# Optimization experiments

Hardware: AMD Instinct MI355X
Metric: run time of the kernel (lower is better)

Reference implementation:

```python
import jax, jax.numpy as jnp
import numpy as np

T, B, D, H = 1024, 128, 256, 256


def setup_inputs() -> dict:
    key = jax.random.key(0)
    ks = jax.random.split(key, 16)
    s_in = 1.0 / np.sqrt(D + H)  # torch Linear default init scale
    inp = {
        "inputs": jax.random.normal(ks[0], (T, B, D), dtype=jnp.float32),
        "Wf": jax.random.uniform(ks[1], (H, D + H), jnp.float32, -s_in, s_in),
        "bf": jax.random.uniform(ks[2], (H,), jnp.float32, -s_in, s_in),
        "Wi": jax.random.uniform(ks[3], (H, D + H), jnp.float32, -s_in, s_in),
        "bi": jax.random.uniform(ks[4], (H,), jnp.float32, -s_in, s_in),
        "Wg": jax.random.uniform(ks[5], (H, D + H), jnp.float32, -s_in, s_in),
        "bg": jax.random.uniform(ks[6], (H,), jnp.float32, -s_in, s_in),
        "Wo": jax.random.uniform(ks[7], (H, D + H), jnp.float32, -s_in, s_in),
        "bo": jax.random.uniform(ks[8], (H,), jnp.float32, -s_in, s_in),
        # estimator params stacked over the 4 gates (order: f, i, g, o)
        "estW1": jax.random.uniform(ks[9], (4, 8, H), jnp.float32, -1/np.sqrt(H), 1/np.sqrt(H)),
        "estb1": jax.random.uniform(ks[10], (4, 8), jnp.float32, -1/np.sqrt(H), 1/np.sqrt(H)),
        "estW2": jax.random.uniform(ks[11], (4, 4, 8), jnp.float32, -1/np.sqrt(8), 1/np.sqrt(8)),
        "estb2": jax.random.uniform(ks[12], (4, 4), jnp.float32, -1/np.sqrt(8), 1/np.sqrt(8)),
        "estW3": jax.random.uniform(ks[13], (4, 1, 4), jnp.float32, -0.5, 0.5),
        "estb3": jax.random.uniform(ks[14], (4, 1), jnp.float32, -0.5, 0.5),
    }
    return inp


def reference(inputs, Wf, bf, Wi, bi, Wg, bg, Wo, bo,
              estW1, estb1, estW2, estb2, estW3, estb3):
    def est(x, k):
        # tiny MLP: H -> 8 -> 4 -> 1 with tanh/tanh/sigmoid
        h1 = jnp.tanh(x @ estW1[k].T + estb1[k])
        h2 = jnp.tanh(h1 @ estW2[k].T + estb2[k])
        return jax.nn.sigmoid(h2 @ estW3[k].T + estb3[k])  # [B, 1]

    def step(carry, x):
        hx, cx = carry
        comb = jnp.concatenate([x, hx], axis=1)  # [B, D+H]
        f = jax.nn.sigmoid(comb @ Wf.T + bf)
        i = jax.nn.sigmoid(comb @ Wi.T + bi)
        g = jnp.tanh(comb @ Wg.T + bg)
        o = jax.nn.sigmoid(comb @ Wo.T + bo)
        f = f * est(f, 0)
        i = i * est(i, 1)
        g = g * est(g, 2)
        o = o * est(o, 3)
        cx = f * cx + i * g
        hx = o * jnp.tanh(cx)
        return (hx, cx), hx

    hx0 = jnp.zeros((B, H), dtype=inputs.dtype)
    cx0 = jnp.zeros((B, H), dtype=inputs.dtype)
    (hx, cx), stacked = jax.lax.scan(step, (hx0, cx0), inputs)
    return stacked, hx, cx
```

## Files before the change

### kernel.cpp

```cpp
#include <hip/hip_runtime.h>
#include <hip/hip_fp16.h>
#include <math.h>

#define T_STEPS 1024
#define BATCH   128
#define D_IN    256
#define H_DIM   256
#define NCOL    1024

typedef _Float16 half2_t __attribute__((ext_vector_type(2)));

__device__ __forceinline__ float sigmoidf_(float x) {
    return 1.0f / (1.0f + __expf(-x));
}

__device__ __forceinline__ float tanhf_(float x) {
    float ax = fabsf(x);
    float t = __expf(-2.0f * ax);
    float r = (1.0f - t) / (1.0f + t);
    return copysignf(r, x);
}

__device__ __forceinline__ float dot2f(unsigned int w, unsigned int h, float acc) {
#if __has_builtin(__builtin_amdgcn_fdot2)
    return __builtin_amdgcn_fdot2(__builtin_bit_cast(half2_t, w),
                                  __builtin_bit_cast(half2_t, h), acc, false);
#else
    __half2 wv = *(__half2*)&w, hv = *(__half2*)&h;
    acc = fmaf(__half2float(wv.x), __half2float(hv.x), acc);
    return fmaf(__half2float(wv.y), __half2float(hv.y), acc);
#endif
}

__device__ __forceinline__ unsigned int packh2(float a, float b) {
    __half2 p = __floats2half2_rn(a, b);
    return *(unsigned int*)&p;
}

__global__ __launch_bounds__(256) void prep_kernel(
    const float* __restrict__ Wf, const float* __restrict__ Wi,
    const float* __restrict__ Wg, const float* __restrict__ Wo,
    const float* __restrict__ bf, const float* __restrict__ bi,
    const float* __restrict__ bg, const float* __restrict__ bo,
    unsigned int* __restrict__ WX2, uint4* __restrict__ WX4,
    uint4* __restrict__ WH4, float* __restrict__ biasc)
{
    int idx = blockIdx.x * 256 + threadIdx.x;
    int m = idx >> 10;
    int j = idx & 1023;
    int g = j >> 8;
    int h = j & 255;
    const float* W = (g == 0) ? Wf : (g == 1) ? Wi : (g == 2) ? Wg : Wo;
    const float* row = W + h * (D_IN + H_DIM);
    const float* rx = row + 8 * m;
    const float* rh = row + D_IN + 8 * m;
    uint4 vx = make_uint4(packh2(rx[0], rx[1]), packh2(rx[2], rx[3]),
                          packh2(rx[4], rx[5]), packh2(rx[6], rx[7]));
    uint4 vh = make_uint4(packh2(rh[0], rh[1]), packh2(rh[2], rh[3]),
                          packh2(rh[4], rh[5]), packh2(rh[6], rh[7]));
    WX4[idx] = vx;
    WH4[idx] = vh;
    unsigned int* d = (unsigned int*)&vx;
    #pragma unroll
    for (int p = 0; p < 4; p++) WX2[(4 * m + p) * 1024 + j] = d[p];
    if (idx < NCOL) {
        const float* bb = (g == 0) ? bf : (g == 1) ? bi : (g == 2) ? bg : bo;
        biasc[j] = bb[h];
    }
}

__global__ __launch_bounds__(256) void pregemm_kernel(
    const float* __restrict__ x, const unsigned int* __restrict__ WX2,
    const float* __restrict__ biasc, float* __restrict__ pre) {
    __shared__ float xs[16 * 256];
    const int tid = threadIdx.x;
    const size_t r0 = (size_t)blockIdx.x * 16;

    {
        const float4* xsrc = (const float4*)(x + r0 * D_IN);
        float4* xd = (float4*)xs;
        #pragma unroll
        for (int i = 0; i < 4; i++) xd[tid + 256 * i] = xsrc[tid + 256 * i];
    }
    float4 b4 = ((const float4*)biasc)[tid];
    float a[16][4];
    #pragma unroll
    for (int r = 0; r < 16; r++) {
        a[r][0] = b4.x; a[r][1] = b4.y; a[r][2] = b4.z; a[r][3] = b4.w;
    }
    __syncthreads();

    const uint4* wp = (const uint4*)WX2;
    const float2* xs2 = (const float2*)xs;
    #pragma unroll 2
    for (int k2 = 0; k2 < 128; k2++) {
        uint4 wv = wp[k2 * 256 + tid];
        __half2 q0 = *(__half2*)&wv.x, q1 = *(__half2*)&wv.y;
        __half2 q2 = *(__half2*)&wv.z, q3 = *(__half2*)&wv.w;
        float w0l = __half2float(q0.x), w0h = __half2float(q0.y);
        float w1l = __half2float(q1.x), w1h = __half2float(q1.y);
        float w2l = __half2float(q2.x), w2h = __half2float(q2.y);
        float w3l = __half2float(q3.x), w3h = __half2float(q3.y);
        #pragma unroll
        for (int r = 0; r < 16; r++) {
            float2 xv = xs2[r * 128 + k2];
            a[r][0] = fmaf(xv.x, w0l, a[r][0]); a[r][0] = fmaf(xv.y, w0h, a[r][0]);
            a[r][1] = fmaf(xv.x, w1l, a[r][1]); a[r][1] = fmaf(xv.y, w1h, a[r][1]);
            a[r][2] = fmaf(xv.x, w2l, a[r][2]); a[r][2] = fmaf(xv.y, w2h, a[r][2]);
            a[r][3] = fmaf(xv.x, w3l, a[r][3]); a[r][3] = fmaf(xv.y, w3h, a[r][3]);
        }
    }
    #pragma unroll
    for (int r = 0; r < 16; r++) {
        ((float4*)(pre + (r0 + r) * NCOL))[tid] =
            make_float4(a[r][0], a[r][1], a[r][2], a[r][3]);
    }
}

__global__ __launch_bounds__(1024) void qlstm_kernel(
    const float* __restrict__ x,
    const uint4* __restrict__ WX4,
    const uint4* __restrict__ WH4,
    const float* __restrict__ biasc,
    const float* __restrict__ pre, int use_pre,
    const float* __restrict__ estW1, const float* __restrict__ estb1,
    const float* __restrict__ estW2, const float* __restrict__ estb2,
    const float* __restrict__ estW3, const float* __restrict__ estb3,
    float* __restrict__ out)
{
    __shared__ __align__(16) __half hxh[H_DIM];
    __shared__ __align__(16) __half hxl[H_DIM];
    __shared__ __align__(16) __half cxh[D_IN];
    __shared__ __align__(16) __half cxl[D_IN];
    __shared__ __align__(16) float gact[NCOL];
    __shared__ float w1[4][8][H_DIM];
    __shared__ float sb1[32];
    __shared__ float sW2[128];
    __shared__ float sb2[16];
    __shared__ float sW3[16];
    __shared__ float sb3[4];
    __shared__ float escale[4];

    const int b    = blockIdx.x;
    const int tid  = threadIdx.x;
    const int w    = tid >> 6;
    const int lane = tid & 63;

    for (int i = tid; i < 4 * 8 * H_DIM; i += 1024) {
        int p = i & 255;
        int base = i & ~255;
        int h = 4 * (p & 63) + (p >> 6);
        ((float*)w1)[i] = estW1[base + h];
    }
    if (tid < 32)  sb1[tid] = estb1[tid];
    if (tid < 128) sW2[tid] = estW2[tid];
    if (tid < 16)  { sb2[tid] = estb2[tid]; sW3[tid] = estW3[tid]; }
    if (tid < 4)   sb3[tid] = estb3[tid];
    if (tid < H_DIM) {
        hxh[tid] = __float2half(0.0f);
        hxl[tid] = __float2half(0.0f);
    }
    float c_reg = 0.0f, h_reg = 0.0f;
    const float b_j = use_pre ? 0.0f : biasc[tid];
    __syncthreads();

    const uint4* hh = (const uint4*)hxh;
    const uint4* hl = (const uint4*)hxl;
    const uint4* xh = (const uint4*)cxh;
    const uint4* xl = (const uint4*)cxl;

    const float* prep_ = pre + (size_t)b * NCOL + tid;
    float pnext = use_pre ? prep_[0] : 0.0f;

    for (int t = 0; t < T_STEPS; t++) {
        float aH, aL = 0.0f;
        if (use_pre) {
            aH = pnext;
            if (t + 1 < T_STEPS)
                pnext = prep_[(size_t)(t + 1) * BATCH * NCOL];
        } else {
            aH = b_j;
            if (tid < D_IN) {
                float xv = x[((size_t)t * BATCH + b) * D_IN + tid];
                __half hi = __float2half_rn(xv);
                cxh[tid] = hi;
                cxl[tid] = __float2half_rn(xv - __half2float(hi));
            }
            __syncthreads();
            #pragma unroll 4
            for (int m = 0; m < 32; m++) {
                uint4 wv = WX4[(m << 10) + tid];
                uint4 hv = xh[m], lv = xl[m];
                aH = dot2f(wv.x, hv.x, aH); aH = dot2f(wv.y, hv.y, aH);
                aH = dot2f(wv.z, hv.z, aH); aH = dot2f(wv.w, hv.w, aH);
                aL = dot2f(wv.x, lv.x, aL); aL = dot2f(wv.y, lv.y, aL);
                aL = dot2f(wv.z, lv.z, aL); aL = dot2f(wv.w, lv.w, aL);
            }
        }

        #pragma unroll 4
        for (int m = 0; m < 32; m++) {
            uint4 wv = WH4[(m << 10) + tid];
            uint4 hv = hh[m], lv = hl[m];
            aH = dot2f(wv.x, hv.x, aH); aH = dot2f(wv.y, hv.y, aH);
            aH = dot2f(wv.z, hv.z, aH); aH = dot2f(wv.w, hv.w, aH);
            aL = dot2f(wv.x, lv.x, aL); aL = dot2f(wv.y, lv.y, aL);
            aL = dot2f(wv.z, lv.z, aL); aL = dot2f(wv.w, lv.w, aL);
        }
        float acc = aH + aL;

        float v = (tid >= 512 && tid < 768) ? tanhf_(acc) : sigmoidf_(acc);
        gact[tid] = v;
        __syncthreads();

        if (tid < 256) {
            float4 gv = ((const float4*)(gact + (w << 8)))[lane];
            float h1[8];
            #pragma unroll
            for (int j = 0; j < 8; j++) {
                const float* wr = &w1[w][j][0];
                float s = fmaf(gv.x, wr[lane],
                          fmaf(gv.y, wr[lane + 64],
                          fmaf(gv.z, wr[lane + 128], gv.w * wr[lane + 192])));
                #pragma unroll
                for (int m2 = 1; m2 < 64; m2 <<= 1) s += __shfl_xor(s, m2, 64);
                h1[j] = tanhf_(s + sb1[w * 8 + j]);
            }
            float h2[4];
            #pragma unroll
            for (int j = 0; j < 4; j++) {
                float s = sb2[w * 4 + j];
                #pragma unroll
                for (int q = 0; q < 8; q++) s = fmaf(h1[q], sW2[w * 32 + j * 8 + q], s);
                h2[j] = tanhf_(s);
            }
            float s3 = sb3[w];
            #pragma unroll
            for (int q = 0; q < 4; q++) s3 = fmaf(h2[q], sW3[w * 4 + q], s3);
            if (lane == 0) escale[w] = sigmoidf_(s3);
        }
        __syncthreads();

        if (tid < 256) {
            float f  = gact[tid]       * escale[0];
            float ii = gact[256 + tid] * escale[1];
            float gg = gact[512 + tid] * escale[2];
            float o  = gact[768 + tid] * escale[3];
            c_reg = fmaf(f, c_reg, ii * gg);
            h_reg = o * tanhf_(c_reg);
            __half hi = __float2half_rn(h_reg);
            hxh[tid] = hi;
            hxl[tid] = __float2half_rn(h_reg - __half2float(hi));
            out[((size_t)t * BATCH + b) * H_DIM + tid] = h_reg;
        }
        __syncthreads();
    }

    if (tid < 256) {
        const size_t stacked = (size_t)T_STEPS * BATCH * H_DIM;
        out[stacked + (size_t)b * H_DIM + tid] = h_reg;
        out[stacked + (size_t)BATCH * H_DIM + (size_t)b * H_DIM + tid] = c_reg;
    }
}

extern "C" void kernel_launch(void* const* d_in, const int* in_sizes, int n_in,
                              void* d_out, int out_size, void* d_ws, size_t ws_size,
                              hipStream_t stream) {
    const float* x     = (const float*)d_in[0];
    const float* Wf    = (const float*)d_in[1];
    const float* bf    = (const float*)d_in[2];
    const float* Wi    = (const float*)d_in[3];
    const float* bi    = (const float*)d_in[4];
    const float* Wg    = (const float*)d_in[5];
    const float* bg    = (const float*)d_in[6];
    const float* Wo    = (const float*)d_in[7];
    const float* bo    = (const float*)d_in[8];
    const float* estW1 = (const float*)d_in[9];
    const float* estb1 = (const float*)d_in[10];
    const float* estW2 = (const float*)d_in[11];
    const float* estb2 = (const float*)d_in[12];
    const float* estW3 = (const float*)d_in[13];
    const float* estb3 = (const float*)d_in[14];

    unsigned int* WX2 = (unsigned int*)d_ws;
    uint4* WX4   = (uint4*)(WX2 + 128 * 1024);
    uint4* WH4   = WX4 + 32 * 1024;
    float* biasc = (float*)(WH4 + 32 * 1024);
    float* pre   = biasc + NCOL;

    const size_t need = (size_t)128 * 1024 * 4 * 3 + NCOL * 4 +
                        (size_t)T_STEPS * BATCH * NCOL * 4;
    const int use_pre = (ws_size >= need) ? 1 : 0;

    prep_kernel<<<128, 256, 0, stream>>>(Wf, Wi, Wg, Wo, bf, bi, bg, bo,
                                         WX2, WX4, WH4, biasc);
    if (use_pre) {
        pregemm_kernel<<<(T_STEPS * BATCH) / 16, 256, 0, stream>>>(x, WX2, biasc, pre);
    }
    qlstm_kernel<<<BATCH, 1024, 0, stream>>>(x, WX4, WH4, biasc, pre, use_pre,
                                             estW1, estb1, estW2, estb2, estW3, estb3,
                                             (float*)d_out);
}
```

Baseline: 10.40 ms.

## Fuse input projection into recurrent kernel, computing chunks of timesteps per block

Removes the separate pregemm kernel and its large T*B*1024 float intermediate buffer. The recurrent kernel now computes the input projection itself for 16 timesteps at once, reading x directly from global memory with the fp16 weights converted to fp32. This is meant to cut the global-memory write and read of the precomputed activations. In exchange it adds redundant per-block work, uncoalesced x loads repeated by all 1024 threads, and 16 extra accumulator registers in a 1024-thread block.

```diff
diff --git a/kernel.cpp b/kernel.cpp
--- a/kernel.cpp
+++ b/kernel.cpp
@@ -7,6 +7,7 @@
 #define D_IN    256
 #define H_DIM   256
 #define NCOL    1024
+#define CH      16
 
 typedef _Float16 half2_t __attribute__((ext_vector_type(2)));
 
@@ -37,13 +38,18 @@
     return *(unsigned int*)&p;
 }
 
+__device__ __forceinline__ uint4 pack8(const float* p) {
+    return make_uint4(packh2(p[0], p[1]), packh2(p[2], p[3]),
+                      packh2(p[4], p[5]), packh2(p[6], p[7]));
+}
+
 __global__ __launch_bounds__(256) void prep_kernel(
     const float* __restrict__ Wf, const float* __restrict__ Wi,
     const float* __restrict__ Wg, const float* __restrict__ Wo,
     const float* __restrict__ bf, const float* __restrict__ bi,
     const float* __restrict__ bg, const float* __restrict__ bo,
-    unsigned int* __restrict__ WX2, uint4* __restrict__ WX4,
-    uint4* __restrict__ WH4, float* __restrict__ biasc)
+    uint4* __restrict__ WX4, uint4* __restrict__ WH4,
+    float* __restrict__ biasc)
 {
     int idx = blockIdx.x * 256 + threadIdx.x;
     int m = idx >> 10;
@@ -52,68 +58,11 @@
     int h = j & 255;
     const float* W = (g == 0) ? Wf : (g == 1) ? Wi : (g == 2) ? Wg : Wo;
     const float* row = W + h * (D_IN + H_DIM);
-    const float* rx = row + 8 * m;
-    const float* rh = row + D_IN + 8 * m;
-    uint4 vx = make_uint4(packh2(rx[0], rx[1]), packh2(rx[2], rx[3]),
-                          packh2(rx[4], rx[5]), packh2(rx[6], rx[7]));
-    uint4 vh = make_uint4(packh2(rh[0], rh[1]), packh2(rh[2], rh[3]),
-                          packh2(rh[4], rh[5]), packh2(rh[6], rh[7]));
-    WX4[idx] = vx;
-    WH4[idx] = vh;
-    unsigned int* d = (unsigned int*)&vx;
-    #pragma unroll
-    for (int p = 0; p < 4; p++) WX2[(4 * m + p) * 1024 + j] = d[p];
+    WX4[idx] = pack8(row + 8 * m);
+    WH4[idx] = pack8(row + D_IN + 8 * m);
     if (idx < NCOL) {
         const float* bb = (g == 0) ? bf : (g == 1) ? bi : (g == 2) ? bg : bo;
-        biasc[j] = bb[h];
-    }
-}
-
-__global__ __launch_bounds__(256) void pregemm_kernel(
-    const float* __restrict__ x, const unsigned int* __restrict__ WX2,
-    const float* __restrict__ biasc, float* __restrict__ pre) {
-    __shared__ float xs[16 * 256];
-    const int tid = threadIdx.x;
-    const size_t r0 = (size_t)blockIdx.x * 16;
-
-    {
-        const float4* xsrc = (const float4*)(x + r0 * D_IN);
-        float4* xd = (float4*)xs;
-        #pragma unroll
-        for (int i = 0; i < 4; i++) xd[tid + 256 * i] = xsrc[tid + 256 * i];
-    }
-    float4 b4 = ((const float4*)biasc)[tid];
-    float a[16][4];
-    #pragma unroll
-    for (int r = 0; r < 16; r++) {
-        a[r][0] = b4.x; a[r][1] = b4.y; a[r][2] = b4.z; a[r][3] = b4.w;
-    }
-    __syncthreads();
-
-    const uint4* wp = (const uint4*)WX2;
-    const float2* xs2 = (const float2*)xs;
-    #pragma unroll 2
-    for (int k2 = 0; k2 < 128; k2++) {
-        uint4 wv = wp[k2 * 256 + tid];
-        __half2 q0 = *(__half2*)&wv.x, q1 = *(__half2*)&wv.y;
-        __half2 q2 = *(__half2*)&wv.z, q3 = *(__half2*)&wv.w;
-        float w0l = __half2float(q0.x), w0h = __half2float(q0.y);
-        float w1l = __half2float(q1.x), w1h = __half2float(q1.y);
-        float w2l = __half2float(q2.x), w2h = __half2float(q2.y);
-        float w3l = __half2float(q3.x), w3h = __half2float(q3.y);
-        #pragma unroll
-        for (int r = 0; r < 16; r++) {
-            float2 xv = xs2[r * 128 + k2];
-            a[r][0] = fmaf(xv.x, w0l, a[r][0]); a[r][0] = fmaf(xv.y, w0h, a[r][0]);
-            a[r][1] = fmaf(xv.x, w1l, a[r][1]); a[r][1] = fmaf(xv.y, w1h, a[r][1]);
-            a[r][2] = fmaf(xv.x, w2l, a[r][2]); a[r][2] = fmaf(xv.y, w2h, a[r][2]);
-            a[r][3] = fmaf(xv.x, w3l, a[r][3]); a[r][3] = fmaf(xv.y, w3h, a[r][3]);
-        }
-    }
-    #pragma unroll
-    for (int r = 0; r < 16; r++) {
-        ((float4*)(pre + (r0 + r) * NCOL))[tid] =
-            make_float4(a[r][0], a[r][1], a[r][2], a[r][3]);
+        biasc[idx] = bb[h];
     }
 }
 
@@ -122,7 +71,6 @@
     const uint4* __restrict__ WX4,
     const uint4* __restrict__ WH4,
     const float* __restrict__ biasc,
-    const float* __restrict__ pre, int use_pre,
     const float* __restrict__ estW1, const float* __restrict__ estb1,
     const float* __restrict__ estW2, const float* __restrict__ estb2,
     const float* __restrict__ estW3, const float* __restrict__ estb3,
@@ -130,10 +78,8 @@
 {
     __shared__ __align__(16) __half hxh[H_DIM];
     __shared__ __align__(16) __half hxl[H_DIM];
-    __shared__ __align__(16) __half cxh[D_IN];
-    __shared__ __align__(16) __half cxl[D_IN];
     __shared__ __align__(16) float gact[NCOL];
-    __shared__ float w1[4][8][H_DIM];
+    __shared__ float w1[4 * 8 * H_DIM];
     __shared__ float sb1[32];
     __shared__ float sW2[128];
     __shared__ float sb2[16];
@@ -150,7 +96,7 @@
         int p = i & 255;
         int base = i & ~255;
         int h = 4 * (p & 63) + (p >> 6);
-        ((float*)w1)[i] = estW1[base + h];
+        w1[i] = estW1[base + h];
     }
     if (tid < 32)  sb1[tid] = estb1[tid];
     if (tid < 128) sW2[tid] = estW2[tid];
@@ -161,99 +107,104 @@
         hxl[tid] = __float2half(0.0f);
     }
     float c_reg = 0.0f, h_reg = 0.0f;
-    const float b_j = use_pre ? 0.0f : biasc[tid];
+    const float b_j = biasc[tid];
     __syncthreads();
 
     const uint4* hh = (const uint4*)hxh;
     const uint4* hl = (const uint4*)hxl;
-    const uint4* xh = (const uint4*)cxh;
-    const uint4* xl = (const uint4*)cxl;
-
-    const float* prep_ = pre + (size_t)b * NCOL + tid;
-    float pnext = use_pre ? prep_[0] : 0.0f;
-
-    for (int t = 0; t < T_STEPS; t++) {
-        float aH, aL = 0.0f;
-        if (use_pre) {
-            aH = pnext;
-            if (t + 1 < T_STEPS)
-                pnext = prep_[(size_t)(t + 1) * BATCH * NCOL];
-        } else {
-            aH = b_j;
-            if (tid < D_IN) {
-                float xv = x[((size_t)t * BATCH + b) * D_IN + tid];
-                __half hi = __float2half_rn(xv);
-                cxh[tid] = hi;
-                cxl[tid] = __float2half_rn(xv - __half2float(hi));
-            }
-            __syncthreads();
+
+    float pacc[CH];
+
+    for (int t0 = 0; t0 < T_STEPS; t0 += CH) {
+        #pragma unroll
+        for (int s = 0; s < CH; s++) pacc[s] = b_j;
+        {
+            const float* xb = x + ((size_t)t0 * BATCH + b) * D_IN;
+            for (int m = 0; m < 32; m++) {
+                uint4 wv = WX4[(m << 10) + tid];
+                __half2 q0 = *(__half2*)&wv.x, q1 = *(__half2*)&wv.y;
+                __half2 q2 = *(__half2*)&wv.z, q3 = *(__half2*)&wv.w;
+                float w0 = __half2float(q0.x), w1f = __half2float(q0.y);
+                float w2 = __half2float(q1.x), w3 = __half2float(q1.y);
+                float w4 = __half2float(q2.x), w5 = __half2float(q2.y);
+                float w6 = __half2float(q3.x), w7 = __half2float(q3.y);
+                #pragma unroll
+                for (int s = 0; s < CH; s++) {
+                    const float* xr = xb + (size_t)s * (BATCH * D_IN) + (m << 3);
+                    float4 xa = *(const float4*)xr;
+                    float4 xc = *(const float4*)(xr + 4);
+                    float a = pacc[s];
+                    a = fmaf(w0, xa.x, a); a = fmaf(w1f, xa.y, a);
+                    a = fmaf(w2, xa.z, a); a = fmaf(w3, xa.w, a);
+                    a = fmaf(w4, xc.x, a); a = fmaf(w5, xc.y, a);
+                    a = fmaf(w6, xc.z, a); a = fmaf(w7, xc.w, a);
+                    pacc[s] = a;
+                }
+            }
+        }
+
+        #pragma unroll 1
+        for (int s = 0; s < CH; s++) {
+            const int t = t0 + s;
+            float aH = pacc[s], aL = 0.0f;
             #pragma unroll 4
             for (int m = 0; m < 32; m++) {
-                uint4 wv = WX4[(m << 10) + tid];
-                uint4 hv = xh[m], lv = xl[m];
+                uint4 wv = WH4[(m << 10) + tid];
+                uint4 hv = hh[m], lv = hl[m];
                 aH = dot2f(wv.x, hv.x, aH); aH = dot2f(wv.y, hv.y, aH);
                 aH = dot2f(wv.z, hv.z, aH); aH = dot2f(wv.w, hv.w, aH);
                 aL = dot2f(wv.x, lv.x, aL); aL = dot2f(wv.y, lv.y, aL);
                 aL = dot2f(wv.z, lv.z, aL); aL = dot2f(wv.w, lv.w, aL);
             }
+            float acc = aH + aL;
+
+            float v = (tid >= 512 && tid < 768) ? tanhf_(acc) : sigmoidf_(acc);
+            gact[tid] = v;
+            __syncthreads();
+
+            if (tid < 256) {
+                float4 gv = ((const float4*)(gact + (w << 8)))[lane];
+                float h1[8];
+                #pragma unroll
+                for (int j = 0; j < 8; j++) {
+                    const float* wr = &w1[(w * 8 + j) * H_DIM];
+                    float sacc = fmaf(gv.x, wr[lane],
+                                 fmaf(gv.y, wr[lane + 64],
+                                 fmaf(gv.z, wr[lane + 128], gv.w * wr[lane + 192])));
+                    #pragma unroll
+                    for (int m2 = 1; m2 < 64; m2 <<= 1) sacc += __shfl_xor(sacc, m2, 64);
+                    h1[j] = tanhf_(sacc + sb1[w * 8 + j]);
+                }
+                float h2[4];
+                #pragma unroll
+                for (int j = 0; j < 4; j++) {
+                    float sacc = sb2[w * 4 + j];
+                    #pragma unroll
+                    for (int q = 0; q < 8; q++)
+                        sacc = fmaf(h1[q], sW2[w * 32 + j * 8 + q], sacc);
+                    h2[j] = tanhf_(sacc);
+                }
+                float s3 = sb3[w];
+                #pragma unroll
+                for (int q = 0; q < 4; q++) s3 = fmaf(h2[q], sW3[w * 4 + q], s3);
+                if (lane == 0) escale[w] = sigmoidf_(s3);
+            }
+            __syncthreads();
+
+            if (tid < 256) {
+                float f  = gact[tid]       * escale[0];
+                float ii = gact[256 + tid] * escale[1];
+                float gg = gact[512 + tid] * escale[2];
+                float o  = gact[768 + tid] * escale[3];
+                c_reg = fmaf(f, c_reg, ii * gg);
+                h_reg = o * tanhf_(c_reg);
+                __half hi = __float2half_rn(h_reg);
+                hxh[tid] = hi;
+                hxl[tid] = __float2half_rn(h_reg - __half2float(hi));
+                out[((size_t)t * BATCH + b) * H_DIM + tid] = h_reg;
+            }
+            __syncthreads();
         }
-
-        #pragma unroll 4
-        for (int m = 0; m < 32; m++) {
-            uint4 wv = WH4[(m << 10) + tid];
-            uint4 hv = hh[m], lv = hl[m];
-            aH = dot2f(wv.x, hv.x, aH); aH = dot2f(wv.y, hv.y, aH);
-            aH = dot2f(wv.z, hv.z, aH); aH = dot2f(wv.w, hv.w, aH);
-            aL = dot2f(wv.x, lv.x, aL); aL = dot2f(wv.y, lv.y, aL);
-            aL = dot2f(wv.z, lv.z, aL); aL = dot2f(wv.w, lv.w, aL);
-        }
-        float acc = aH + aL;
-
-        float v = (tid >= 512 && tid < 768) ? tanhf_(acc) : sigmoidf_(acc);
-        gact[tid] = v;
-        __syncthreads();
-
-        if (tid < 256) {
-            float4 gv = ((const float4*)(gact + (w << 8)))[lane];
-            float h1[8];
-            #pragma unroll
-            for (int j = 0; j < 8; j++) {
-                const float* wr = &w1[w][j][0];
-                float s = fmaf(gv.x, wr[lane],
-                          fmaf(gv.y, wr[lane + 64],
-                          fmaf(gv.z, wr[lane + 128], gv.w * wr[lane + 192])));
-                #pragma unroll
-                for (int m2 = 1; m2 < 64; m2 <<= 1) s += __shfl_xor(s, m2, 64);
-                h1[j] = tanhf_(s + sb1[w * 8 + j]);
-            }
-            float h2[4];
-            #pragma unroll
-            for (int j = 0; j < 4; j++) {
-                float s = sb2[w * 4 + j];
-                #pragma unroll
-                for (int q = 0; q < 8; q++) s = fmaf(h1[q], sW2[w * 32 + j * 8 + q], s);
-                h2[j] = tanhf_(s);
-            }
-            float s3 = sb3[w];
-            #pragma unroll
-            for (int q = 0; q < 4; q++) s3 = fmaf(h2[q], sW3[w * 4 + q], s3);
-            if (lane == 0) escale[w] = sigmoidf_(s3);
-        }
-        __syncthreads();
-
-        if (tid < 256) {
-            float f  = gact[tid]       * escale[0];
-            float ii = gact[256 + tid] * escale[1];
-            float gg = gact[512 + tid] * escale[2];
-            float o  = gact[768 + tid] * escale[3];
-            c_reg = fmaf(f, c_reg, ii * gg);
-            h_reg = o * tanhf_(c_reg);
-            __half hi = __float2half_rn(h_reg);
-            hxh[tid] = hi;
-            hxl[tid] = __float2half_rn(h_reg - __half2float(hi));
-            out[((size_t)t * BATCH + b) * H_DIM + tid] = h_reg;
-        }
-        __syncthreads();
     }
 
     if (tid < 256) {
@@ -282,22 +233,13 @@
     const float* estW3 = (const float*)d_in[13];
     const float* estb3 = (const float*)d_in[14];
 
-    unsigned int* WX2 = (unsigned int*)d_ws;
-    uint4* WX4   = (uint4*)(WX2 + 128 * 1024);
-    uint4* WH4   = WX4 + 32 * 1024;
-    float* biasc = (float*)(WH4 + 32 * 1024);
-    float* pre   = biasc + NCOL;
-
-    const size_t need = (size_t)128 * 1024 * 4 * 3 + NCOL * 4 +
-                        (size_t)T_STEPS * BATCH * NCOL * 4;
-    const int use_pre = (ws_size >= need) ? 1 : 0;
+    uint4* WX4   = (uint4*)d_ws;
+    uint4* WH4   = WX4 + 32768;
+    float* biasc = (float*)(WH4 + 32768);
 
     prep_kernel<<<128, 256, 0, stream>>>(Wf, Wi, Wg, Wo, bf, bi, bg, bo,
-                                         WX2, WX4, WH4, biasc);
-    if (use_pre) {
-        pregemm_kernel<<<(T_STEPS * BATCH) / 16, 256, 0, stream>>>(x, WX2, biasc, pre);
-    }
-    qlstm_kernel<<<BATCH, 1024, 0, stream>>>(x, WX4, WH4, biasc, pre, use_pre,
-                                             estW1, estb1, estW2, estb2, estW3, estb3,
-                                             (float*)d_out);
-}
+                                         WX4, WH4, biasc);
+    qlstm_kernel<<<BATCH, 1024, 0, stream>>>(
+        x, WX4, WH4, biasc,
+        estW1, estb1, estW2, estb2, estW3, estb3, (float*)d_out);
+}
```

New measurement: 10.64 ms. 2.3% more time.
